# Optimization experiments

Hardware: AMD Instinct MI355X
Metric: run time of the kernel (lower is better)

The kernel has to match this reference:

```python
import jax, jax.numpy as jnp
import numpy as np

B, T, C = 64, 256, 64
E, H, HB, OUT = 32, 64, 128, 2


def setup_inputs() -> dict:
    key = jax.random.key(0)
    ks = iter(jax.random.split(key, 32))
    s = 0.02
    p = {}
    p["x"] = jax.random.normal(next(ks), (B, T, C), jnp.float32)
    # embedding Linear(1, E)
    p["embed_w"] = jax.random.normal(next(ks), (E, 1), jnp.float32) * s
    p["embed_b"] = jnp.zeros((E,), jnp.float32)
    # GRU (input E, hidden H); gate order r,z,n
    p["w_ih"] = jax.random.normal(next(ks), (3 * H, E), jnp.float32) * s
    p["w_hh"] = jax.random.normal(next(ks), (3 * H, H), jnp.float32) * s
    p["b_ih"] = jnp.zeros((3 * H,), jnp.float32)
    p["b_hh"] = jnp.zeros((3 * H,), jnp.float32)
    # BTP query / key MLPs: H->HB->HB->HB
    for nm in ("q", "k"):
        p[f"{nm}1_w"] = jax.random.normal(next(ks), (HB, H), jnp.float32) * s
        p[f"{nm}1_b"] = jnp.zeros((HB,), jnp.float32)
        p[f"{nm}2_w"] = jax.random.normal(next(ks), (HB, HB), jnp.float32) * s
        p[f"{nm}2_b"] = jnp.zeros((HB,), jnp.float32)
        p[f"{nm}3_w"] = jax.random.normal(next(ks), (HB, HB), jnp.float32) * s
        p[f"{nm}3_b"] = jnp.zeros((HB,), jnp.float32)
    # Gate bias (n_components x n_components), torch.randn init
    p["gate_bias"] = jax.random.normal(next(ks), (C, C), jnp.float32)
    # classifier: C^2 -> C^2/2 -> C^2/4 -> OUT
    d0, d1, d2 = C * C, C * C // 2, C * C // 4
    p["clf1_w"] = jax.random.normal(next(ks), (d1, d0), jnp.float32) * s
    p["clf1_b"] = jnp.zeros((d1,), jnp.float32)
    p["clf2_w"] = jax.random.normal(next(ks), (d2, d1), jnp.float32) * s
    p["clf2_b"] = jnp.zeros((d2,), jnp.float32)
    p["clf3_w"] = jax.random.normal(next(ks), (OUT, d2), jnp.float32) * s
    p["clf3_b"] = jnp.zeros((OUT,), jnp.float32)
    # predictor Linear(H, 1)
    p["pred_w"] = jax.random.normal(next(ks), (1, H), jnp.float32) * s
    p["pred_b"] = jnp.zeros((1,), jnp.float32)
    return p


def _mlp3(h, w1, b1, w2, b2, w3, b3):
    h = jax.nn.relu(h @ w1.T + b1)
    h = jax.nn.relu(h @ w2.T + b2)
    return h @ w3.T + b3


def reference(x, embed_w, embed_b, w_ih, w_hh, b_ih, b_hh,
              q1_w, q1_b, q2_w, q2_b, q3_w, q3_b,
              k1_w, k1_b, k2_w, k2_b, k3_w, k3_b,
              gate_bias, clf1_w, clf1_b, clf2_w, clf2_b, clf3_w, clf3_b,
              pred_w, pred_b):
    Bb, Tt, Cc = x.shape
    Hh = w_hh.shape[1]
    # embeddings: Linear(1,E) applied to each scalar -> [B,C,T,E]
    embedded = x.transpose(0, 2, 1)[..., None] * embed_w[:, 0] + embed_b
    xs = jnp.moveaxis(embedded, 2, 0)  # [T,B,C,E]

    def gru_cell(h, xt):
        gi = xt @ w_ih.T + b_ih           # [B,C,3H]
        gh = h @ w_hh.T + b_hh
        gi_r, gi_z, gi_n = jnp.split(gi, 3, axis=-1)
        gh_r, gh_z, gh_n = jnp.split(gh, 3, axis=-1)
        r = jax.nn.sigmoid(gi_r + gh_r)
        z = jax.nn.sigmoid(gi_z + gh_z)
        n = jnp.tanh(gi_n + r * gh_n)
        return (1.0 - z) * n + z * h

    def btp(h):
        q = _mlp3(h, q1_w, q1_b, q2_w, q2_b, q3_w, q3_b)   # [B,C,HB]
        k = _mlp3(h, k1_w, k1_b, k2_w, k2_b, k3_w, k3_b)
        transfer = jnp.einsum('bqd,bkd->bqk', q, k)        # [B,C,C]
        norms = jnp.sqrt(jnp.sum(transfer * transfer, axis=(1, 2), keepdims=True))
        transfer = transfer / norms
        gate = jax.nn.sigmoid(jnp.abs(transfer) + gate_bias)
        transfer = transfer * gate
        next_states = jnp.einsum('bij,bjd->bid', transfer, h)
        return next_states, transfer

    def step(h, xt):
        h = gru_cell(h, xt)
        h, transfer = btp(h)
        return h, (h, transfer)

    h0 = jnp.zeros((Bb, Cc, Hh), x.dtype)
    _, (hs, mats) = jax.lax.scan(step, h0, xs)
    hidden_states = jnp.moveaxis(hs, 0, 1)    # [B,T,C,H]
    matrices = jnp.moveaxis(mats, 0, 1)       # [B,T,C,C]

    # predictor on hidden states at t=0..T-2 -> predicts x[:,1:,:]
    predicted = (hidden_states[:, :-1] @ pred_w.T + pred_b)[..., 0]  # [B,T-1,C]

    clf_in = matrices.reshape(Bb, Tt, Cc * Cc)
    h1 = jax.nn.relu(clf_in @ clf1_w.T + clf1_b)   # dropout is identity in eval
    h2 = jax.nn.relu(h1 @ clf2_w.T + clf2_b)
    time_logits = h2 @ clf3_w.T + clf3_b            # [B,T,OUT]
    logits = jnp.mean(time_logits, axis=1)          # [B,OUT]
    return logits, matrices, time_logits, predicted, x[:, 1:, :]
```

## Files before the change

kernel.cpp:

```cpp
#include <hip/hip_runtime.h>
#include <math.h>

#define B_BATCH 64
#define T_STEPS 256
#define C_COMP  64

#define WSW_BYTE_OFF 2048
#define WHH_OFF 0
#define Q1_OFF 12288
#define K1_OFF 20480
#define Q2_OFF 28672
#define K2_OFF 45056
#define Q3_OFF 61440
#define K3_OFF 77824
#define C1WB_BYTE 262144
#define C2WB_BYTE 17039360
#define H1B_BYTE  21233664
#define H2B_BYTE  88342528

#define MAT_OFF  128
#define TL_OFF   67108992
#define PRED_OFF 67141760
#define XC_OFF   68186240

typedef __attribute__((ext_vector_type(8))) short short8;
typedef __attribute__((ext_vector_type(4))) float f32x4;
#define MFMA16(a,b,c) __builtin_amdgcn_mfma_f32_16x16x32_bf16(a,b,c,0,0,0)

__device__ __forceinline__ float sigm(float v) { return 1.0f / (1.0f + expf(-v)); }
__device__ __forceinline__ float tanh_f(float v) {
    float e = expf(2.0f * v);
    return 1.0f - 2.0f / (e + 1.0f);
}
__device__ __forceinline__ short f2bf(float f) {
    unsigned u = __float_as_uint(f);
    u += 0x7fffu + ((u >> 16) & 1u);
    return (short)(u >> 16);
}
__device__ __forceinline__ float bf2f(short s) {
    return __uint_as_float(((unsigned)(unsigned short)s) << 16);
}
__device__ __forceinline__ void async16(void* lds, const void* g) {
    __builtin_amdgcn_global_load_lds((const __attribute__((address_space(1))) void*)g,
                                     (__attribute__((address_space(3))) void*)lds, 16, 0, 0);
}

__global__ void precompute_kernel(const float* __restrict__ w_ih,
                                  const float* __restrict__ embed_w,
                                  const float* __restrict__ embed_b,
                                  const float* __restrict__ b_ih,
                                  float* __restrict__ avec, float* __restrict__ cvec)
{
    int g = threadIdx.x;
    if (g < 192) {
        float a = 0.f, c = 0.f;
        for (int e = 0; e < 32; ++e) {
            float w = w_ih[g * 32 + e];
            a += w * embed_w[e];
            c += w * embed_b[e];
        }
        avec[g] = a;
        cvec[g] = c + b_ih[g];
    }
}

__global__ void tobf16_kernel(const float* __restrict__ src, short* __restrict__ dst, int n)
{
    int i = blockIdx.x * 256 + threadIdx.x;
    if (i < n) dst[i] = f2bf(src[i]);
}

template<int KST, bool RELU>
__device__ __forceinline__ void two_strip_layer(
    const short* __restrict__ A, const int ast,
    const short8* __restrict__ Bs0, const short8* __restrict__ Bs1,
    const float bias0, const float bias1,
    short* __restrict__ outb, const int ost,
    const int s0, const int s1, const int ln, const int lh)
{
    f32x4 acc0[4], acc1[4];
#pragma unroll
    for (int m = 0; m < 4; ++m) {
        acc0[m] = (f32x4){bias0, bias0, bias0, bias0};
        acc1[m] = (f32x4){bias1, bias1, bias1, bias1};
    }
#pragma unroll
    for (int kk = 0; kk < KST; ++kk) {
#pragma unroll
        for (int m = 0; m < 4; ++m) {
            short8 a = *(const short8*)&A[(m * 16 + ln) * ast + kk * 32 + lh * 8];
            acc0[m] = MFMA16(a, Bs0[kk], acc0[m]);
            acc1[m] = MFMA16(a, Bs1[kk], acc1[m]);
        }
    }
#pragma unroll
    for (int m = 0; m < 4; ++m) {
#pragma unroll
        for (int q = 0; q < 4; ++q) {
            const int row = m * 16 + lh * 4 + q;
            float v0 = acc0[m][q], v1 = acc1[m][q];
            if (RELU) { v0 = fmaxf(v0, 0.f); v1 = fmaxf(v1, 0.f); }
            outb[row * ost + s0 * 16 + ln] = f2bf(v0);
            outb[row * ost + s1 * 16 + ln] = f2bf(v1);
        }
    }
}

__global__ __launch_bounds__(512) void scan_kernel(
    const float* __restrict__ x, const float* __restrict__ b_hh,
    const float* __restrict__ avec, const float* __restrict__ cvec,
    const short* __restrict__ wsw,
    const float* __restrict__ q1b, const float* __restrict__ q2b, const float* __restrict__ q3b,
    const float* __restrict__ k1b, const float* __restrict__ k2b, const float* __restrict__ k3b,
    const float* __restrict__ gate_bias,
    const float* __restrict__ pred_w, const float* __restrict__ pred_b,
    float* __restrict__ matrices, float* __restrict__ predicted)
{
    __shared__ __align__(16) float h32[64 * 67];
    __shared__ __align__(16) short hb [64 * 72];
    __shared__ __align__(16) short hbT[64 * 72];
    __shared__ __align__(16) short qf [64 * 136];
    __shared__ __align__(16) short kf [64 * 136];
    __shared__ __align__(16) char scratch[69632];
    __shared__ float avec_s[192], cvec_s[192], bhh_s[192], pw_s[64], xrow[64], red[8];

    float* gates = (float*)scratch;
    short* act1q = (short*)scratch;
    short* act1k = (short*)(scratch + 17408);
    short* act2q = (short*)(scratch + 34816);
    short* act2k = (short*)(scratch + 52224);
    float* tf    = (float*)scratch;
    short* tb    = (short*)(scratch + 17408);

    const int tid = threadIdx.x;
    const int b = blockIdx.x;
    const int w = tid >> 6, lane = tid & 63;
    const int ln = lane & 15, lh = lane >> 4;
    const int wq = w & 3;

    for (int i = tid; i < 64 * 67; i += 512) h32[i] = 0.f;
    for (int i = tid; i < 64 * 72; i += 512) hb[i] = 0;
    if (tid < 192) { avec_s[tid] = avec[tid]; cvec_s[tid] = cvec[tid]; bhh_s[tid] = b_hh[tid]; }
    if (tid < 64) pw_s[tid] = pred_w[tid];
    const float pbv = pred_b[0];

    const short* whh_b = wsw + WHH_OFF;
    const short* l1w = (w < 4) ? wsw + Q1_OFF : wsw + K1_OFF;
    const short* l2w = (w < 4) ? wsw + Q2_OFF : wsw + K2_OFF;
    const short* l3w = (w < 4) ? wsw + Q3_OFF : wsw + K3_OFF;
    const float* l1b = (w < 4) ? q1b : k1b;
    const float* l2b = (w < 4) ? q2b : k2b;
    const float* l3b = (w < 4) ? q3b : k3b;

    short8 Bg[2][2], B1[2][2], B2[2][4], B3[2][4];
    {
        const int sg1 = (w < 4) ? (w + 8) : w;
#pragma unroll
        for (int kk = 0; kk < 2; ++kk) {
            Bg[0][kk] = *(const short8*)&whh_b[(w   * 16 + ln) * 64 + kk * 32 + lh * 8];
            Bg[1][kk] = *(const short8*)&whh_b[(sg1 * 16 + ln) * 64 + kk * 32 + lh * 8];
        }
#pragma unroll
        for (int s = 0; s < 2; ++s) {
            const int strip = wq + s * 4;
#pragma unroll
            for (int kk = 0; kk < 2; ++kk)
                B1[s][kk] = *(const short8*)&l1w[(strip * 16 + ln) * 64 + kk * 32 + lh * 8];
#pragma unroll
            for (int kk = 0; kk < 4; ++kk) {
                B2[s][kk] = *(const short8*)&l2w[(strip * 16 + ln) * 128 + kk * 32 + lh * 8];
                B3[s][kk] = *(const short8*)&l3w[(strip * 16 + ln) * 128 + kk * 32 + lh * 8];
            }
        }
    }
    const float b1v0 = l1b[wq * 16 + ln],       b1v1 = l1b[(wq + 4) * 16 + ln];
    const float b2v0 = l2b[wq * 16 + ln],       b2v1 = l2b[(wq + 4) * 16 + ln];
    const float b3v0 = l3b[wq * 16 + ln],       b3v1 = l3b[(wq + 4) * 16 + ln];
    __syncthreads();

    for (int t = 0; t < T_STEPS; ++t) {
        {
            f32x4 a0[4], a1[4];
#pragma unroll
            for (int m = 0; m < 4; ++m) { a0[m] = (f32x4){0,0,0,0}; a1[m] = (f32x4){0,0,0,0}; }
#pragma unroll
            for (int kk = 0; kk < 2; ++kk)
#pragma unroll
                for (int m = 0; m < 4; ++m) {
                    short8 av = *(const short8*)&hb[(m * 16 + ln) * 72 + kk * 32 + lh * 8];
                    a0[m] = MFMA16(av, Bg[0][kk], a0[m]);
                    a1[m] = MFMA16(av, Bg[1][kk], a1[m]);
                }
#pragma unroll
            for (int m = 0; m < 4; ++m)
#pragma unroll
                for (int q = 0; q < 4; ++q)
                    gates[(m * 16 + lh * 4 + q) * 193 + w * 16 + ln] = a0[m][q];
            if (w < 4) {
#pragma unroll
                for (int m = 0; m < 4; ++m)
#pragma unroll
                    for (int q = 0; q < 4; ++q)
                        gates[(m * 16 + lh * 4 + q) * 193 + (w + 8) * 16 + ln] = a1[m][q];
            }
        }
        if (tid < 64) xrow[tid] = x[((size_t)b * T_STEPS + t) * 64 + tid];
        __syncthreads();

        {
            const int c = tid >> 3, j0 = (tid & 7) * 8;
            const float xv = xrow[c];
#pragma unroll
            for (int jj = 0; jj < 8; ++jj) {
                const int j = j0 + jj;
                const float ghr = gates[c * 193 + j]       + bhh_s[j];
                const float ghz = gates[c * 193 + 64 + j]  + bhh_s[64 + j];
                const float ghn = gates[c * 193 + 128 + j] + bhh_s[128 + j];
                const float r = sigm(fmaf(xv, avec_s[j],        cvec_s[j])        + ghr);
                const float z = sigm(fmaf(xv, avec_s[64 + j],   cvec_s[64 + j])   + ghz);
                const float n = tanh_f(fmaf(xv, avec_s[128 + j], cvec_s[128 + j]) + r * ghn);
                const float hold = h32[c * 67 + j];
                const float hn = fmaf(z, hold - n, n);
                h32[c * 67 + j] = hn;
                const short hv = f2bf(hn);
                hb[c * 72 + j] = hv;
                hbT[j * 72 + c] = hv;
            }
        }
        __syncthreads();

        short* o1 = (w < 4) ? act1q : act1k;
        two_strip_layer<2, true >(hb, 72, B1[0], B1[1], b1v0, b1v1, o1, 136, wq, wq + 4, ln, lh);
        __syncthreads();
        short* o2 = (w < 4) ? act2q : act2k;
        two_strip_layer<4, true >(o1, 136, B2[0], B2[1], b2v0, b2v1, o2, 136, wq, wq + 4, ln, lh);
        __syncthreads();
        short* o3 = (w < 4) ? qf : kf;
        two_strip_layer<4, false>(o2, 136, B3[0], B3[1], b3v0, b3v1, o3, 136, wq, wq + 4, ln, lh);
        __syncthreads();

        {
            const int m = wq, n0 = w >> 2;
            f32x4 ac0 = {0,0,0,0}, ac1 = {0,0,0,0};
#pragma unroll
            for (int kk = 0; kk < 4; ++kk) {
                short8 av = *(const short8*)&qf[(m * 16 + ln) * 136 + kk * 32 + lh * 8];
                short8 b0 = *(const short8*)&kf[(n0 * 16 + ln) * 136 + kk * 32 + lh * 8];
                short8 b1 = *(const short8*)&kf[((n0 + 2) * 16 + ln) * 136 + kk * 32 + lh * 8];
                ac0 = MFMA16(av, b0, ac0);
                ac1 = MFMA16(av, b1, ac1);
            }
            float ss = 0.f;
#pragma unroll
            for (int q = 0; q < 4; ++q) {
                const int row = m * 16 + lh * 4 + q;
                tf[row * 67 + n0 * 16 + ln] = ac0[q];
                tf[row * 67 + (n0 + 2) * 16 + ln] = ac1[q];
                ss = fmaf(ac0[q], ac0[q], fmaf(ac1[q], ac1[q], ss));
            }
#pragma unroll
            for (int off = 1; off < 64; off <<= 1) ss += __shfl_xor(ss, off);
            if (lane == 0) red[w] = ss;
        }
        __syncthreads();

        {
            const float ssum = red[0]+red[1]+red[2]+red[3]+red[4]+red[5]+red[6]+red[7];
            const float inv = 1.0f / sqrtf(ssum);
            const size_t mbase = ((size_t)b * T_STEPS + t) * 4096;
#pragma unroll
            for (int it = 0; it < 8; ++it) {
                const int e = it * 512 + tid;
                const int ci = e >> 6, cj = e & 63;
                const float tv = tf[ci * 67 + cj] * inv;
                const float g = sigm(fabsf(tv) + gate_bias[e]);
                const float val = tv * g;
                matrices[mbase + e] = val;
                tb[ci * 72 + cj] = f2bf(val);
            }
        }
        __syncthreads();

        {
            const int m = wq, n0 = w >> 2;
            f32x4 ac0 = {0,0,0,0}, ac1 = {0,0,0,0};
#pragma unroll
            for (int kk = 0; kk < 2; ++kk) {
                short8 av = *(const short8*)&tb[(m * 16 + ln) * 72 + kk * 32 + lh * 8];
                short8 b0 = *(const short8*)&hbT[(n0 * 16 + ln) * 72 + kk * 32 + lh * 8];
                short8 b1 = *(const short8*)&hbT[((n0 + 2) * 16 + ln) * 72 + kk * 32 + lh * 8];
                ac0 = MFMA16(av, b0, ac0);
                ac1 = MFMA16(av, b1, ac1);
            }
#pragma unroll
            for (int q = 0; q < 4; ++q) {
                const int row = m * 16 + lh * 4 + q;
                const int c0 = n0 * 16 + ln;
                h32[row * 67 + c0]      = ac0[q];
                h32[row * 67 + c0 + 32] = ac1[q];
                hb[row * 72 + c0]       = f2bf(ac0[q]);
                hb[row * 72 + c0 + 32]  = f2bf(ac1[q]);
            }
        }
        __syncthreads();

        if (t < T_STEPS - 1) {
            const int c = tid >> 3, jj = tid & 7;
            float p = 0.f;
#pragma unroll
            for (int u = 0; u < 8; ++u) p = fmaf(h32[c * 67 + jj * 8 + u], pw_s[jj * 8 + u], p);
            p += __shfl_xor(p, 1); p += __shfl_xor(p, 2); p += __shfl_xor(p, 4);
            if (jj == 0) predicted[((size_t)b * (T_STEPS - 1) + t) * 64 + c] = p + pbv;
        }
    }
}

__global__ void copyx_kernel(const float* __restrict__ x, float* __restrict__ out5)
{
    int i = blockIdx.x * 256 + threadIdx.x;
    if (i < B_BATCH * (T_STEPS - 1) * C_COMP) {
        int b = i / ((T_STEPS - 1) * C_COMP);
        int r = i - b * (T_STEPS - 1) * C_COMP;
        out5[i] = x[(size_t)b * (T_STEPS * C_COMP) + r + C_COMP];
    }
}

__global__ __launch_bounds__(256) void gemm1_kernel(
    const float* __restrict__ A, const short* __restrict__ Bw,
    const float* __restrict__ bias, short* __restrict__ Cb,
    const int M, const int N, const int K)
{
    __shared__ __align__(16) short Asb[128 * 64];
    __shared__ __align__(16) short Bsb[128 * 64];
    const int tid = threadIdx.x;
    const int w = tid >> 6, lane = tid & 63;
    const int ln = lane & 15, lh = lane >> 4;
    const int wr = w >> 1, wc = w & 1;

    const int ntc = N >> 7;
    const int g = blockIdx.x;
    const int xcd = g & 7, chunk = g >> 3;
    const int mt = xcd * ((M >> 7) >> 3) + chunk / ntc;
    const int nt = chunk % ntc;
    const int m0 = mt << 7, n0 = nt << 7;

    const int ar = tid >> 1;
    const int ac = (tid & 1) << 5;
    const short* bsrc = Bw + (size_t)(n0 + w * 32 + (lane >> 3)) * K + ((lane & 7) << 3);
    short* bdst = &Bsb[w * 32 * 64 + lane * 8];

    f32x4 acc[4][4];
#pragma unroll
    for (int m = 0; m < 4; ++m)
#pragma unroll
        for (int n = 0; n < 4; ++n) acc[m][n] = (f32x4){0, 0, 0, 0};

    for (int k0 = 0; k0 < K; k0 += 64) {
        const float* arow = A + (size_t)(m0 + ar) * K + k0 + ac;
        float4 av[8];
#pragma unroll
        for (int i = 0; i < 8; ++i) av[i] = *reinterpret_cast<const float4*>(arow + i * 4);
        short8 cv[4];
#pragma unroll
        for (int i = 0; i < 4; ++i) {
            cv[i][0] = f2bf(av[2*i].x);   cv[i][1] = f2bf(av[2*i].y);
            cv[i][2] = f2bf(av[2*i].z);   cv[i][3] = f2bf(av[2*i].w);
            cv[i][4] = f2bf(av[2*i+1].x); cv[i][5] = f2bf(av[2*i+1].y);
            cv[i][6] = f2bf(av[2*i+1].z); cv[i][7] = f2bf(av[2*i+1].w);
        }
        __syncthreads();
#pragma unroll
        for (int i = 0; i < 4; ++i)
            *reinterpret_cast<short8*>(&Asb[ar * 64 + ac + i * 8]) = cv[i];
#pragma unroll
        for (int i = 0; i < 4; ++i)
            async16(bdst + i * 512, bsrc + (size_t)i * 8 * K + k0);
        __syncthreads();
#pragma unroll
        for (int kk = 0; kk < 2; ++kk) {
            short8 af[4], bfr[4];
#pragma unroll
            for (int m = 0; m < 4; ++m)
                af[m] = *reinterpret_cast<const short8*>(&Asb[(wr*64 + m*16 + ln)*64 + kk*32 + lh*8]);
#pragma unroll
            for (int n = 0; n < 4; ++n)
                bfr[n] = *reinterpret_cast<const short8*>(&Bsb[(wc*64 + n*16 + ln)*64 + kk*32 + lh*8]);
#pragma unroll
            for (int m = 0; m < 4; ++m)
#pragma unroll
                for (int n = 0; n < 4; ++n)
                    acc[m][n] = MFMA16(af[m], bfr[n], acc[m][n]);
        }
    }
#pragma unroll
    for (int n = 0; n < 4; ++n) {
        const int col = n0 + wc * 64 + n * 16 + ln;
        const float bv = bias[col];
#pragma unroll
        for (int m = 0; m < 4; ++m)
#pragma unroll
            for (int q = 0; q < 4; ++q) {
                const int row = m0 + wr * 64 + m * 16 + lh * 4 + q;
                Cb[(size_t)row * N + col] = f2bf(fmaxf(acc[m][n][q] + bv, 0.f));
            }
    }
}

__global__ __launch_bounds__(256) void gemm2_kernel(
    const short* __restrict__ Ab, const short* __restrict__ Bw,
    const float* __restrict__ bias, short* __restrict__ Cb,
    const int M, const int N, const int K)
{
    __shared__ __align__(16) short Asb[128 * 64];
    __shared__ __align__(16) short Bsb[128 * 64];
    const int tid = threadIdx.x;
    const int w = tid >> 6, lane = tid & 63;
    const int ln = lane & 15, lh = lane >> 4;
    const int wr = w >> 1, wc = w & 1;

    const int ntc = N >> 7;
    const int g = blockIdx.x;
    const int xcd = g & 7, chunk = g >> 3;
    const int mt = xcd * ((M >> 7) >> 3) + chunk / ntc;
    const int nt = chunk % ntc;
    const int m0 = mt << 7, n0 = nt << 7;

    const short* asrc = Ab + (size_t)(m0 + w * 32 + (lane >> 3)) * K + ((lane & 7) << 3);
    const short* bsrc = Bw + (size_t)(n0 + w * 32 + (lane >> 3)) * K + ((lane & 7) << 3);
    short* adst = &Asb[w * 32 * 64 + lane * 8];
    short* bdst = &Bsb[w * 32 * 64 + lane * 8];

    f32x4 acc[4][4];
#pragma unroll
    for (int m = 0; m < 4; ++m)
#pragma unroll
        for (int n = 0; n < 4; ++n) acc[m][n] = (f32x4){0, 0, 0, 0};

    for (int k0 = 0; k0 < K; k0 += 64) {
        __syncthreads();
#pragma unroll
        for (int i = 0; i < 4; ++i) {
            async16(adst + i * 512, asrc + (size_t)i * 8 * K + k0);
            async16(bdst + i * 512, bsrc + (size_t)i * 8 * K + k0);
        }
        __syncthreads();
#pragma unroll
        for (int kk = 0; kk < 2; ++kk) {
            short8 af[4], bfr[4];
#pragma unroll
            for (int m = 0; m < 4; ++m)
                af[m] = *reinterpret_cast<const short8*>(&Asb[(wr*64 + m*16 + ln)*64 + kk*32 + lh*8]);
#pragma unroll
            for (int n = 0; n < 4; ++n)
                bfr[n] = *reinterpret_cast<const short8*>(&Bsb[(wc*64 + n*16 + ln)*64 + kk*32 + lh*8]);
#pragma unroll
            for (int m = 0; m < 4; ++m)
#pragma unroll
                for (int n = 0; n < 4; ++n)
                    acc[m][n] = MFMA16(af[m], bfr[n], acc[m][n]);
        }
    }
#pragma unroll
    for (int n = 0; n < 4; ++n) {
        const int col = n0 + wc * 64 + n * 16 + ln;
        const float bv = bias[col];
#pragma unroll
        for (int m = 0; m < 4; ++m)
#pragma unroll
            for (int q = 0; q < 4; ++q) {
                const int row = m0 + wr * 64 + m * 16 + lh * 4 + q;
                Cb[(size_t)row * N + col] = f2bf(fmaxf(acc[m][n][q] + bv, 0.f));
            }
    }
}

__global__ __launch_bounds__(256) void clf3_kernel(const short* __restrict__ h2b,
    const float* __restrict__ w3, const float* __restrict__ b3, float* __restrict__ TL)
{
    const int lane = threadIdx.x & 63;
    const int w = threadIdx.x >> 6;
    const size_t r = (size_t)blockIdx.x * 4 + w;
    const short* hr = h2b + r * 1024;
    float a0 = 0.f, a1 = 0.f;
#pragma unroll
    for (int half = 0; half < 2; ++half) {
        const int k = half * 512 + lane * 8;
        short8 hv = *(const short8*)&hr[k];
#pragma unroll
        for (int u = 0; u < 8; ++u) {
            const float hf = bf2f(hv[u]);
            a0 = fmaf(hf, w3[k + u], a0);
            a1 = fmaf(hf, w3[1024 + k + u], a1);
        }
    }
    for (int off = 32; off; off >>= 1) { a0 += __shfl_xor(a0, off); a1 += __shfl_xor(a1, off); }
    if (lane == 0) {
        TL[r * 2 + 0] = a0 + b3[0];
        TL[r * 2 + 1] = a1 + b3[1];
    }
}

__global__ void logits_kernel(const float* __restrict__ TL, float* __restrict__ out)
{
    const int tid = threadIdx.x;
    if (tid >= 128) return;
    const int b = tid >> 1, o = tid & 1;
    float s = 0.f;
    for (int t = 0; t < T_STEPS; ++t) s += TL[((size_t)b * T_STEPS + t) * 2 + o];
    out[b * 2 + o] = s * (1.0f / 256.0f);
}

extern "C" void kernel_launch(void* const* d_in, const int* in_sizes, int n_in,
                              void* d_out, int out_size, void* d_ws, size_t ws_size,
                              hipStream_t stream)
{
    const float* x       = (const float*)d_in[0];
    const float* embed_w = (const float*)d_in[1];
    const float* embed_b = (const float*)d_in[2];
    const float* w_ih    = (const float*)d_in[3];
    const float* w_hh    = (const float*)d_in[4];
    const float* b_ih    = (const float*)d_in[5];
    const float* b_hh    = (const float*)d_in[6];
    const float* q1w = (const float*)d_in[7],  *q1b = (const float*)d_in[8];
    const float* q2w = (const float*)d_in[9],  *q2b = (const float*)d_in[10];
    const float* q3w = (const float*)d_in[11], *q3b = (const float*)d_in[12];
    const float* k1w = (const float*)d_in[13], *k1b = (const float*)d_in[14];
    const float* k2w = (const float*)d_in[15], *k2b = (const float*)d_in[16];
    const float* k3w = (const float*)d_in[17], *k3b = (const float*)d_in[18];
    const float* gate_bias = (const float*)d_in[19];
    const float* c1w = (const float*)d_in[20], *c1b = (const float*)d_in[21];
    const float* c2w = (const float*)d_in[22], *c2b = (const float*)d_in[23];
    const float* c3w = (const float*)d_in[24], *c3b = (const float*)d_in[25];
    const float* pw  = (const float*)d_in[26], *pb  = (const float*)d_in[27];

    float* out       = (float*)d_out;
    float* logits    = out;
    float* matrices  = out + MAT_OFF;
    float* TL        = out + TL_OFF;
    float* predicted = out + PRED_OFF;
    float* xcopy     = out + XC_OFF;

    float* ws   = (float*)d_ws;
    float* avec = ws;
    float* cvec = ws + 192;
    short* wsw  = (short*)((char*)d_ws + WSW_BYTE_OFF);
    short* c1wb = (short*)((char*)d_ws + C1WB_BYTE);
    short* c2wb = (short*)((char*)d_ws + C2WB_BYTE);
    short* h1b  = (short*)((char*)d_ws + H1B_BYTE);
    short* h2b  = (short*)((char*)d_ws + H2B_BYTE);

    precompute_kernel<<<1, 256, 0, stream>>>(w_ih, embed_w, embed_b, b_ih, avec, cvec);

    tobf16_kernel<<<(12288 + 255) / 256, 256, 0, stream>>>(w_hh, wsw + WHH_OFF, 12288);
    tobf16_kernel<<<(8192  + 255) / 256, 256, 0, stream>>>(q1w,  wsw + Q1_OFF,  8192);
    tobf16_kernel<<<(8192  + 255) / 256, 256, 0, stream>>>(k1w,  wsw + K1_OFF,  8192);
    tobf16_kernel<<<(16384 + 255) / 256, 256, 0, stream>>>(q2w,  wsw + Q2_OFF,  16384);
    tobf16_kernel<<<(16384 + 255) / 256, 256, 0, stream>>>(k2w,  wsw + K2_OFF,  16384);
    tobf16_kernel<<<(16384 + 255) / 256, 256, 0, stream>>>(q3w,  wsw + Q3_OFF,  16384);
    tobf16_kernel<<<(16384 + 255) / 256, 256, 0, stream>>>(k3w,  wsw + K3_OFF,  16384);
    tobf16_kernel<<<(2048 * 4096 + 255) / 256, 256, 0, stream>>>(c1w, c1wb, 2048 * 4096);
    tobf16_kernel<<<(1024 * 2048 + 255) / 256, 256, 0, stream>>>(c2w, c2wb, 1024 * 2048);

    scan_kernel<<<B_BATCH, 512, 0, stream>>>(x, b_hh, avec, cvec, wsw,
        q1b, q2b, q3b, k1b, k2b, k3b, gate_bias, pw, pb, matrices, predicted);

    copyx_kernel<<<(B_BATCH * (T_STEPS - 1) * C_COMP + 255) / 256, 256, 0, stream>>>(x, xcopy);

    const int Mtot = B_BATCH * T_STEPS;
    gemm1_kernel<<<(Mtot / 128) * (2048 / 128), 256, 0, stream>>>(
        matrices, c1wb, c1b, h1b, Mtot, 2048, 4096);
    gemm2_kernel<<<(Mtot / 128) * (1024 / 128), 256, 0, stream>>>(
        h1b, c2wb, c2b, h2b, Mtot, 1024, 2048);
    clf3_kernel<<<Mtot / 4, 256, 0, stream>>>(h2b, c3w, c3b, TL);
    logits_kernel<<<1, 128, 0, stream>>>(TL, logits);
}
```

Measured before the change: 3.262 ms.

## Widen scan kernel to 1024 threads, swizzle LDS, emit bf16 matrices for GEMM1

The recurrent scan kernel now runs 16 waves instead of 8, so each wave handles one MFMA strip instead of two. Padded LDS layouts are replaced with XOR-swizzled ones. The predictor dot product moves to the start of the next step, and sigmoid/tanh/rsqrt use fast hardware intrinsics. When the workspace is large enough, the scan also writes a bf16 copy of the matrices, so the first classifier GEMM can use the bf16-input kernel instead of converting fp32 on load. This adds extra global writes and more synchronisation pressure across a 1024-thread block.

After: 3.533 ms. +8.3%, slower.

```diff
diff --git a/kernel.cpp b/kernel.cpp
--- a/kernel.cpp
+++ b/kernel.cpp
@@ -1,4 +1,5 @@
 #include <hip/hip_runtime.h>
+#include <hip/hip_bf16.h>
 #include <math.h>
 
 #define B_BATCH 64
@@ -17,6 +18,7 @@
 #define C2WB_BYTE 17039360
 #define H1B_BYTE  21233664
 #define H2B_BYTE  88342528
+#define MB16_BYTE 121896960ULL
 
 #define MAT_OFF  128
 #define TL_OFF   67108992
@@ -24,21 +26,29 @@
 #define XC_OFF   68186240
 
 typedef __attribute__((ext_vector_type(8))) short short8;
+typedef __attribute__((ext_vector_type(4))) short short4v;
 typedef __attribute__((ext_vector_type(4))) float f32x4;
 #define MFMA16(a,b,c) __builtin_amdgcn_mfma_f32_16x16x32_bf16(a,b,c,0,0,0)
 
-__device__ __forceinline__ float sigm(float v) { return 1.0f / (1.0f + expf(-v)); }
-__device__ __forceinline__ float tanh_f(float v) {
-    float e = expf(2.0f * v);
-    return 1.0f - 2.0f / (e + 1.0f);
-}
-__device__ __forceinline__ short f2bf(float f) {
+__device__ __forceinline__ float fsigm(float v) {
+    return __builtin_amdgcn_rcpf(1.0f + __expf(-v));
+}
+__device__ __forceinline__ float ftanh(float v) {
+    return 1.0f - 2.0f * __builtin_amdgcn_rcpf(__expf(2.0f * v) + 1.0f);
+}
+__device__ __forceinline__ short f2bs(float f) {
     unsigned u = __float_as_uint(f);
     u += 0x7fffu + ((u >> 16) & 1u);
     return (short)(u >> 16);
 }
 __device__ __forceinline__ float bf2f(short s) {
     return __uint_as_float(((unsigned)(unsigned short)s) << 16);
+}
+__device__ __forceinline__ int swz64(int row, int col) {
+    return row * 64 + (col ^ (((row >> 1) & 7) << 3));
+}
+__device__ __forceinline__ int swz128(int row, int col) {
+    return row * 128 + (col ^ (((row >> 1) & 7) << 3));
 }
 __device__ __forceinline__ void async16(void* lds, const void* g) {
     __builtin_amdgcn_global_load_lds((const __attribute__((address_space(1))) void*)g,
@@ -67,46 +77,38 @@
 __global__ void tobf16_kernel(const float* __restrict__ src, short* __restrict__ dst, int n)
 {
     int i = blockIdx.x * 256 + threadIdx.x;
-    if (i < n) dst[i] = f2bf(src[i]);
-}
-
-template<int KST, bool RELU>
-__device__ __forceinline__ void two_strip_layer(
-    const short* __restrict__ A, const int ast,
-    const short8* __restrict__ Bs0, const short8* __restrict__ Bs1,
-    const float bias0, const float bias1,
-    short* __restrict__ outb, const int ost,
-    const int s0, const int s1, const int ln, const int lh)
-{
-    f32x4 acc0[4], acc1[4];
-#pragma unroll
-    for (int m = 0; m < 4; ++m) {
-        acc0[m] = (f32x4){bias0, bias0, bias0, bias0};
-        acc1[m] = (f32x4){bias1, bias1, bias1, bias1};
-    }
-#pragma unroll
-    for (int kk = 0; kk < KST; ++kk) {
+    if (i < n) dst[i] = f2bs(src[i]);
+}
+
+template<int KST, int AST, bool RELU>
+__device__ __forceinline__ void layerK(const short* __restrict__ A,
+                                       const short8* __restrict__ Bf, const float bias,
+                                       short* __restrict__ outb,
+                                       const int s, const int ln, const int lh)
+{
+    f32x4 acc[4];
+#pragma unroll
+    for (int m = 0; m < 4; ++m) acc[m] = (f32x4){bias, bias, bias, bias};
+#pragma unroll
+    for (int kk = 0; kk < KST; ++kk)
 #pragma unroll
         for (int m = 0; m < 4; ++m) {
-            short8 a = *(const short8*)&A[(m * 16 + ln) * ast + kk * 32 + lh * 8];
-            acc0[m] = MFMA16(a, Bs0[kk], acc0[m]);
-            acc1[m] = MFMA16(a, Bs1[kk], acc1[m]);
-        }
-    }
-#pragma unroll
-    for (int m = 0; m < 4; ++m) {
+            const int row = m * 16 + ln;
+            short8 a = *(const short8*)&A[row * AST + ((kk * 32 + lh * 8) ^ (((row >> 1) & 7) << 3))];
+            acc[m] = MFMA16(a, Bf[kk], acc[m]);
+        }
+#pragma unroll
+    for (int m = 0; m < 4; ++m)
 #pragma unroll
         for (int q = 0; q < 4; ++q) {
             const int row = m * 16 + lh * 4 + q;
-            float v0 = acc0[m][q], v1 = acc1[m][q];
-            if (RELU) { v0 = fmaxf(v0, 0.f); v1 = fmaxf(v1, 0.f); }
-            outb[row * ost + s0 * 16 + ln] = f2bf(v0);
-            outb[row * ost + s1 * 16 + ln] = f2bf(v1);
-        }
-    }
-}
-
-__global__ __launch_bounds__(512) void scan_kernel(
+            float v = acc[m][q];
+            if (RELU) v = fmaxf(v, 0.f);
+            outb[swz128(row, s * 16 + ln)] = f2bs(v);
+        }
+}
+
+__global__ __launch_bounds__(1024) void scan_kernel(
     const float* __restrict__ x, const float* __restrict__ b_hh,
     const float* __restrict__ avec, const float* __restrict__ cvec,
     const short* __restrict__ wsw,
@@ -114,204 +116,189 @@
     const float* __restrict__ k1b, const float* __restrict__ k2b, const float* __restrict__ k3b,
     const float* __restrict__ gate_bias,
     const float* __restrict__ pred_w, const float* __restrict__ pred_b,
-    float* __restrict__ matrices, float* __restrict__ predicted)
+    float* __restrict__ matrices, float* __restrict__ predicted,
+    short* __restrict__ mb16, const int use_mb16)
 {
     __shared__ __align__(16) float h32[64 * 67];
-    __shared__ __align__(16) short hb [64 * 72];
-    __shared__ __align__(16) short hbT[64 * 72];
-    __shared__ __align__(16) short qf [64 * 136];
-    __shared__ __align__(16) short kf [64 * 136];
-    __shared__ __align__(16) char scratch[69632];
-    __shared__ float avec_s[192], cvec_s[192], bhh_s[192], pw_s[64], xrow[64], red[8];
-
-    float* gates = (float*)scratch;
-    short* act1q = (short*)scratch;
-    short* act1k = (short*)(scratch + 17408);
-    short* act2q = (short*)(scratch + 34816);
-    short* act2k = (short*)(scratch + 52224);
-    float* tf    = (float*)scratch;
-    short* tb    = (short*)(scratch + 17408);
+    __shared__ __align__(16) short hb [64 * 64];
+    __shared__ __align__(16) short hbT[64 * 64];
+    __shared__ __align__(16) short qf [64 * 128];
+    __shared__ __align__(16) short kf [64 * 128];
+    __shared__ __align__(16) char arena[65536];
+    __shared__ float avec_s[192], cvec_s[192], bhh_s[192], pw_s[64], xrow[64], red[16];
+
+    short* act1q = (short*)arena;
+    short* act1k = (short*)(arena + 16384);
+    short* act2q = (short*)(arena + 32768);
+    short* act2k = (short*)(arena + 49152);
+    float* gates = (float*)arena;
+    float* tf    = (float*)arena;
+    short* tb    = (short*)(arena + 17408);
 
     const int tid = threadIdx.x;
     const int b = blockIdx.x;
     const int w = tid >> 6, lane = tid & 63;
     const int ln = lane & 15, lh = lane >> 4;
-    const int wq = w & 3;
-
-    for (int i = tid; i < 64 * 67; i += 512) h32[i] = 0.f;
-    for (int i = tid; i < 64 * 72; i += 512) hb[i] = 0;
+    const int path = w >> 3;
+    const int w8 = w & 7;
+
+    for (int i = tid; i < 64 * 67; i += 1024) h32[i] = 0.f;
+    for (int i = tid; i < 64 * 64; i += 1024) { hb[i] = 0; hbT[i] = 0; }
     if (tid < 192) { avec_s[tid] = avec[tid]; cvec_s[tid] = cvec[tid]; bhh_s[tid] = b_hh[tid]; }
     if (tid < 64) pw_s[tid] = pred_w[tid];
     const float pbv = pred_b[0];
 
     const short* whh_b = wsw + WHH_OFF;
-    const short* l1w = (w < 4) ? wsw + Q1_OFF : wsw + K1_OFF;
-    const short* l2w = (w < 4) ? wsw + Q2_OFF : wsw + K2_OFF;
-    const short* l3w = (w < 4) ? wsw + Q3_OFF : wsw + K3_OFF;
-    const float* l1b = (w < 4) ? q1b : k1b;
-    const float* l2b = (w < 4) ? q2b : k2b;
-    const float* l3b = (w < 4) ? q3b : k3b;
-
-    short8 Bg[2][2], B1[2][2], B2[2][4], B3[2][4];
-    {
-        const int sg1 = (w < 4) ? (w + 8) : w;
-#pragma unroll
-        for (int kk = 0; kk < 2; ++kk) {
-            Bg[0][kk] = *(const short8*)&whh_b[(w   * 16 + ln) * 64 + kk * 32 + lh * 8];
-            Bg[1][kk] = *(const short8*)&whh_b[(sg1 * 16 + ln) * 64 + kk * 32 + lh * 8];
-        }
-#pragma unroll
-        for (int s = 0; s < 2; ++s) {
-            const int strip = wq + s * 4;
+    const short* l1w = path ? wsw + K1_OFF : wsw + Q1_OFF;
+    const short* l2w = path ? wsw + K2_OFF : wsw + Q2_OFF;
+    const short* l3w = path ? wsw + K3_OFF : wsw + Q3_OFF;
+    const float* l1b = path ? k1b : q1b;
+    const float* l2b = path ? k2b : q2b;
+    const float* l3b = path ? k3b : q3b;
+
+    short8 Bg[2], B1[2], B2[4], B3[4];
+    if (w < 12) {
+#pragma unroll
+        for (int kk = 0; kk < 2; ++kk)
+            Bg[kk] = *(const short8*)&whh_b[(w * 16 + ln) * 64 + kk * 32 + lh * 8];
+    }
+#pragma unroll
+    for (int kk = 0; kk < 2; ++kk)
+        B1[kk] = *(const short8*)&l1w[(w8 * 16 + ln) * 64 + kk * 32 + lh * 8];
+#pragma unroll
+    for (int kk = 0; kk < 4; ++kk) {
+        B2[kk] = *(const short8*)&l2w[(w8 * 16 + ln) * 128 + kk * 32 + lh * 8];
+        B3[kk] = *(const short8*)&l3w[(w8 * 16 + ln) * 128 + kk * 32 + lh * 8];
+    }
+    const float b1v = l1b[w8 * 16 + ln];
+    const float b2v = l2b[w8 * 16 + ln];
+    const float b3v = l3b[w8 * 16 + ln];
+    __syncthreads();
+
+    for (int t = 0; t < T_STEPS; ++t) {
+        if (t > 0) {
+            const int c = tid >> 4, jj = tid & 15;
+            float p = 0.f;
+#pragma unroll
+            for (int u = 0; u < 4; ++u) p = fmaf(h32[c * 67 + jj * 4 + u], pw_s[jj * 4 + u], p);
+            p += __shfl_xor(p, 1); p += __shfl_xor(p, 2);
+            p += __shfl_xor(p, 4); p += __shfl_xor(p, 8);
+            if (jj == 0) predicted[((size_t)b * (T_STEPS - 1) + (t - 1)) * 64 + c] = p + pbv;
+        }
+        if (w < 12) {
+            f32x4 a[4];
+#pragma unroll
+            for (int m = 0; m < 4; ++m) a[m] = (f32x4){0, 0, 0, 0};
 #pragma unroll
             for (int kk = 0; kk < 2; ++kk)
-                B1[s][kk] = *(const short8*)&l1w[(strip * 16 + ln) * 64 + kk * 32 + lh * 8];
-#pragma unroll
-            for (int kk = 0; kk < 4; ++kk) {
-                B2[s][kk] = *(const short8*)&l2w[(strip * 16 + ln) * 128 + kk * 32 + lh * 8];
-                B3[s][kk] = *(const short8*)&l3w[(strip * 16 + ln) * 128 + kk * 32 + lh * 8];
-            }
-        }
-    }
-    const float b1v0 = l1b[wq * 16 + ln],       b1v1 = l1b[(wq + 4) * 16 + ln];
-    const float b2v0 = l2b[wq * 16 + ln],       b2v1 = l2b[(wq + 4) * 16 + ln];
-    const float b3v0 = l3b[wq * 16 + ln],       b3v1 = l3b[(wq + 4) * 16 + ln];
-    __syncthreads();
-
-    for (int t = 0; t < T_STEPS; ++t) {
+#pragma unroll
+                for (int m = 0; m < 4; ++m) {
+                    const int row = m * 16 + ln;
+                    short8 av = *(const short8*)&hb[swz64(row, kk * 32 + lh * 8)];
+                    a[m] = MFMA16(av, Bg[kk], a[m]);
+                }
+#pragma unroll
+            for (int m = 0; m < 4; ++m)
+#pragma unroll
+                for (int q = 0; q < 4; ++q)
+                    gates[(m * 16 + lh * 4 + q) * 193 + w * 16 + ln] = a[m][q];
+        }
+        if (w == 15) xrow[lane] = x[((size_t)b * T_STEPS + t) * 64 + lane];
+        __syncthreads();
+
         {
-            f32x4 a0[4], a1[4];
-#pragma unroll
-            for (int m = 0; m < 4; ++m) { a0[m] = (f32x4){0,0,0,0}; a1[m] = (f32x4){0,0,0,0}; }
-#pragma unroll
-            for (int kk = 0; kk < 2; ++kk)
-#pragma unroll
-                for (int m = 0; m < 4; ++m) {
-                    short8 av = *(const short8*)&hb[(m * 16 + ln) * 72 + kk * 32 + lh * 8];
-                    a0[m] = MFMA16(av, Bg[0][kk], a0[m]);
-                    a1[m] = MFMA16(av, Bg[1][kk], a1[m]);
-                }
-#pragma unroll
-            for (int m = 0; m < 4; ++m)
-#pragma unroll
-                for (int q = 0; q < 4; ++q)
-                    gates[(m * 16 + lh * 4 + q) * 193 + w * 16 + ln] = a0[m][q];
-            if (w < 4) {
-#pragma unroll
-                for (int m = 0; m < 4; ++m)
-#pragma unroll
-                    for (int q = 0; q < 4; ++q)
-                        gates[(m * 16 + lh * 4 + q) * 193 + (w + 8) * 16 + ln] = a1[m][q];
-            }
-        }
-        if (tid < 64) xrow[tid] = x[((size_t)b * T_STEPS + t) * 64 + tid];
-        __syncthreads();
-
-        {
-            const int c = tid >> 3, j0 = (tid & 7) * 8;
+            const int c = tid >> 4, jseg = (tid & 15) * 4;
             const float xv = xrow[c];
-#pragma unroll
-            for (int jj = 0; jj < 8; ++jj) {
-                const int j = j0 + jj;
+            short4v hv4;
+#pragma unroll
+            for (int jj = 0; jj < 4; ++jj) {
+                const int j = jseg + jj;
                 const float ghr = gates[c * 193 + j]       + bhh_s[j];
                 const float ghz = gates[c * 193 + 64 + j]  + bhh_s[64 + j];
                 const float ghn = gates[c * 193 + 128 + j] + bhh_s[128 + j];
-                const float r = sigm(fmaf(xv, avec_s[j],        cvec_s[j])        + ghr);
-                const float z = sigm(fmaf(xv, avec_s[64 + j],   cvec_s[64 + j])   + ghz);
-                const float n = tanh_f(fmaf(xv, avec_s[128 + j], cvec_s[128 + j]) + r * ghn);
+                const float r = fsigm(fmaf(xv, avec_s[j],        cvec_s[j])        + ghr);
+                const float z = fsigm(fmaf(xv, avec_s[64 + j],   cvec_s[64 + j])   + ghz);
+                const float n = ftanh(fmaf(xv, avec_s[128 + j], cvec_s[128 + j]) + r * ghn);
                 const float hold = h32[c * 67 + j];
                 const float hn = fmaf(z, hold - n, n);
                 h32[c * 67 + j] = hn;
-                const short hv = f2bf(hn);
-                hb[c * 72 + j] = hv;
-                hbT[j * 72 + c] = hv;
-            }
-        }
-        __syncthreads();
-
-        short* o1 = (w < 4) ? act1q : act1k;
-        two_strip_layer<2, true >(hb, 72, B1[0], B1[1], b1v0, b1v1, o1, 136, wq, wq + 4, ln, lh);
-        __syncthreads();
-        short* o2 = (w < 4) ? act2q : act2k;
-        two_strip_layer<4, true >(o1, 136, B2[0], B2[1], b2v0, b2v1, o2, 136, wq, wq + 4, ln, lh);
-        __syncthreads();
-        short* o3 = (w < 4) ? qf : kf;
-        two_strip_layer<4, false>(o2, 136, B3[0], B3[1], b3v0, b3v1, o3, 136, wq, wq + 4, ln, lh);
+                const short hv = f2bs(hn);
+                hv4[jj] = hv;
+                hbT[swz64(j, c)] = hv;
+            }
+            *(short4v*)&hb[c * 64 + (jseg ^ (((c >> 1) & 7) << 3))] = hv4;
+        }
+        __syncthreads();
+
+        layerK<2, 64,  true >(hb, B1, b1v, path ? act1k : act1q, w8, ln, lh);
+        __syncthreads();
+        layerK<4, 128, true >(path ? act1k : act1q, B2, b2v, path ? act2k : act2q, w8, ln, lh);
+        __syncthreads();
+        layerK<4, 128, false>(path ? act2k : act2q, B3, b3v, path ? kf : qf, w8, ln, lh);
         __syncthreads();
 
         {
-            const int m = wq, n0 = w >> 2;
-            f32x4 ac0 = {0,0,0,0}, ac1 = {0,0,0,0};
+            const int m = w >> 2, n = w & 3;
+            f32x4 ac = {0, 0, 0, 0};
 #pragma unroll
             for (int kk = 0; kk < 4; ++kk) {
-                short8 av = *(const short8*)&qf[(m * 16 + ln) * 136 + kk * 32 + lh * 8];
-                short8 b0 = *(const short8*)&kf[(n0 * 16 + ln) * 136 + kk * 32 + lh * 8];
-                short8 b1 = *(const short8*)&kf[((n0 + 2) * 16 + ln) * 136 + kk * 32 + lh * 8];
-                ac0 = MFMA16(av, b0, ac0);
-                ac1 = MFMA16(av, b1, ac1);
+                const int rq = m * 16 + ln, rk = n * 16 + ln;
+                short8 a  = *(const short8*)&qf[swz128(rq, kk * 32 + lh * 8)];
+                short8 bm = *(const short8*)&kf[swz128(rk, kk * 32 + lh * 8)];
+                ac = MFMA16(a, bm, ac);
             }
             float ss = 0.f;
+#pragma unroll
+            for (int q = 0; q < 4; ++q) {
+                tf[(m * 16 + lh * 4 + q) * 67 + n * 16 + ln] = ac[q];
+                ss = fmaf(ac[q], ac[q], ss);
+            }
+#pragma unroll
+            for (int off = 1; off < 64; off <<= 1) ss += __shfl_xor(ss, off);
+            if (lane == 0) red[w] = ss;
+        }
+        __syncthreads();
+
+        {
+            float ssum = 0.f;
+#pragma unroll
+            for (int i = 0; i < 16; ++i) ssum += red[i];
+            const float inv = __builtin_amdgcn_rsqf(ssum);
+            const size_t mbase = ((size_t)b * T_STEPS + t) * 4096;
+#pragma unroll
+            for (int it = 0; it < 4; ++it) {
+                const int e = it * 1024 + tid;
+                const int ci = e >> 6, cj = e & 63;
+                const float tv = tf[ci * 67 + cj] * inv;
+                const float g = fsigm(fabsf(tv) + gate_bias[e]);
+                const float val = tv * g;
+                matrices[mbase + e] = val;
+                const short vb = f2bs(val);
+                if (use_mb16) mb16[mbase + e] = vb;
+                tb[swz64(ci, cj)] = vb;
+            }
+        }
+        __syncthreads();
+
+        {
+            const int m = w >> 2, n = w & 3;
+            f32x4 ac = {0, 0, 0, 0};
+#pragma unroll
+            for (int kk = 0; kk < 2; ++kk) {
+                const int ra = m * 16 + ln, rbm = n * 16 + ln;
+                short8 a  = *(const short8*)&tb [swz64(ra,  kk * 32 + lh * 8)];
+                short8 bm = *(const short8*)&hbT[swz64(rbm, kk * 32 + lh * 8)];
+                ac = MFMA16(a, bm, ac);
+            }
 #pragma unroll
             for (int q = 0; q < 4; ++q) {
                 const int row = m * 16 + lh * 4 + q;
-                tf[row * 67 + n0 * 16 + ln] = ac0[q];
-                tf[row * 67 + (n0 + 2) * 16 + ln] = ac1[q];
-                ss = fmaf(ac0[q], ac0[q], fmaf(ac1[q], ac1[q], ss));
-            }
-#pragma unroll
-            for (int off = 1; off < 64; off <<= 1) ss += __shfl_xor(ss, off);
-            if (lane == 0) red[w] = ss;
-        }
-        __syncthreads();
-
-        {
-            const float ssum = red[0]+red[1]+red[2]+red[3]+red[4]+red[5]+red[6]+red[7];
-            const float inv = 1.0f / sqrtf(ssum);
-            const size_t mbase = ((size_t)b * T_STEPS + t) * 4096;
-#pragma unroll
-            for (int it = 0; it < 8; ++it) {
-                const int e = it * 512 + tid;
-                const int ci = e >> 6, cj = e & 63;
-                const float tv = tf[ci * 67 + cj] * inv;
-                const float g = sigm(fabsf(tv) + gate_bias[e]);
-                const float val = tv * g;
-                matrices[mbase + e] = val;
-                tb[ci * 72 + cj] = f2bf(val);
-            }
-        }
-        __syncthreads();
-
-        {
-            const int m = wq, n0 = w >> 2;
-            f32x4 ac0 = {0,0,0,0}, ac1 = {0,0,0,0};
-#pragma unroll
-            for (int kk = 0; kk < 2; ++kk) {
-                short8 av = *(const short8*)&tb[(m * 16 + ln) * 72 + kk * 32 + lh * 8];
-                short8 b0 = *(const short8*)&hbT[(n0 * 16 + ln) * 72 + kk * 32 + lh * 8];
-                short8 b1 = *(const short8*)&hbT[((n0 + 2) * 16 + ln) * 72 + kk * 32 + lh * 8];
-                ac0 = MFMA16(av, b0, ac0);
-                ac1 = MFMA16(av, b1, ac1);
-            }
-#pragma unroll
-            for (int q = 0; q < 4; ++q) {
-                const int row = m * 16 + lh * 4 + q;
-                const int c0 = n0 * 16 + ln;
-                h32[row * 67 + c0]      = ac0[q];
-                h32[row * 67 + c0 + 32] = ac1[q];
-                hb[row * 72 + c0]       = f2bf(ac0[q]);
-                hb[row * 72 + c0 + 32]  = f2bf(ac1[q]);
-            }
-        }
-        __syncthreads();
-
-        if (t < T_STEPS - 1) {
-            const int c = tid >> 3, jj = tid & 7;
-            float p = 0.f;
-#pragma unroll
-            for (int u = 0; u < 8; ++u) p = fmaf(h32[c * 67 + jj * 8 + u], pw_s[jj * 8 + u], p);
-            p += __shfl_xor(p, 1); p += __shfl_xor(p, 2); p += __shfl_xor(p, 4);
-            if (jj == 0) predicted[((size_t)b * (T_STEPS - 1) + t) * 64 + c] = p + pbv;
-        }
+                const int col = n * 16 + ln;
+                h32[row * 67 + col] = ac[q];
+                hb[swz64(row, col)] = f2bs(ac[q]);
+            }
+        }
+        __syncthreads();
     }
 }
 
@@ -363,10 +350,10 @@
         short8 cv[4];
 #pragma unroll
         for (int i = 0; i < 4; ++i) {
-            cv[i][0] = f2bf(av[2*i].x);   cv[i][1] = f2bf(av[2*i].y);
-            cv[i][2] = f2bf(av[2*i].z);   cv[i][3] = f2bf(av[2*i].w);
-            cv[i][4] = f2bf(av[2*i+1].x); cv[i][5] = f2bf(av[2*i+1].y);
-            cv[i][6] = f2bf(av[2*i+1].z); cv[i][7] = f2bf(av[2*i+1].w);
+            cv[i][0] = f2bs(av[2*i].x);   cv[i][1] = f2bs(av[2*i].y);
+            cv[i][2] = f2bs(av[2*i].z);   cv[i][3] = f2bs(av[2*i].w);
+            cv[i][4] = f2bs(av[2*i+1].x); cv[i][5] = f2bs(av[2*i+1].y);
+            cv[i][6] = f2bs(av[2*i+1].z); cv[i][7] = f2bs(av[2*i+1].w);
         }
         __syncthreads();
 #pragma unroll
@@ -401,7 +388,7 @@
 #pragma unroll
             for (int q = 0; q < 4; ++q) {
                 const int row = m0 + wr * 64 + m * 16 + lh * 4 + q;
-                Cb[(size_t)row * N + col] = f2bf(fmaxf(acc[m][n][q] + bv, 0.f));
+                Cb[(size_t)row * N + col] = f2bs(fmaxf(acc[m][n][q] + bv, 0.f));
             }
     }
 }
@@ -469,7 +456,7 @@
 #pragma unroll
             for (int q = 0; q < 4; ++q) {
                 const int row = m0 + wr * 64 + m * 16 + lh * 4 + q;
-                Cb[(size_t)row * N + col] = f2bf(fmaxf(acc[m][n][q] + bv, 0.f));
+                Cb[(size_t)row * N + col] = f2bs(fmaxf(acc[m][n][q] + bv, 0.f));
             }
     }
 }
@@ -549,6 +536,9 @@
     short* h1b  = (short*)((char*)d_ws + H1B_BYTE);
     short* h2b  = (short*)((char*)d_ws + H2B_BYTE);
 
+    const int use_mb16 = (ws_size >= MB16_BYTE + 134217728ULL) ? 1 : 0;
+    short* mb16 = use_mb16 ? (short*)((char*)d_ws + MB16_BYTE) : (short*)d_ws;
+
     precompute_kernel<<<1, 256, 0, stream>>>(w_ih, embed_w, embed_b, b_ih, avec, cvec);
 
     tobf16_kernel<<<(12288 + 255) / 256, 256, 0, stream>>>(w_hh, wsw + WHH_OFF, 12288);
@@ -561,14 +551,20 @@
     tobf16_kernel<<<(2048 * 4096 + 255) / 256, 256, 0, stream>>>(c1w, c1wb, 2048 * 4096);
     tobf16_kernel<<<(1024 * 2048 + 255) / 256, 256, 0, stream>>>(c2w, c2wb, 1024 * 2048);
 
-    scan_kernel<<<B_BATCH, 512, 0, stream>>>(x, b_hh, avec, cvec, wsw,
-        q1b, q2b, q3b, k1b, k2b, k3b, gate_bias, pw, pb, matrices, predicted);
+    scan_kernel<<<B_BATCH, 1024, 0, stream>>>(x, b_hh, avec, cvec, wsw,
+        q1b, q2b, q3b, k1b, k2b, k3b, gate_bias, pw, pb, matrices, predicted,
+        mb16, use_mb16);
 
     copyx_kernel<<<(B_BATCH * (T_STEPS - 1) * C_COMP + 255) / 256, 256, 0, stream>>>(x, xcopy);
 
     const int Mtot = B_BATCH * T_STEPS;
-    gemm1_kernel<<<(Mtot / 128) * (2048 / 128), 256, 0, stream>>>(
-        matrices, c1wb, c1b, h1b, Mtot, 2048, 4096);
+    if (use_mb16) {
+        gemm2_kernel<<<(Mtot / 128) * (2048 / 128), 256, 0, stream>>>(
+            mb16, c1wb, c1b, h1b, Mtot, 2048, 4096);
+    } else {
+        gemm1_kernel<<<(Mtot / 128) * (2048 / 128), 256, 0, stream>>>(
+            matrices, c1wb, c1b, h1b, Mtot, 2048, 4096);
+    }
     gemm2_kernel<<<(Mtot / 128) * (1024 / 128), 256, 0, stream>>>(
         h1b, c2wb, c2b, h2b, Mtot, 1024, 2048);
     clf3_kernel<<<Mtot / 4, 256, 0, stream>>>(h2b, c3w, c3b, TL);
```
